# Performance work log

Measured on AMD Instinct MI355X. Metric: run time of the kernel, lower is better.

## Reference

```python
import jax, jax.numpy as jnp
import numpy as np

B, C, H, W = 32, 512, 32, 32  # in_dims = token_dim = 512, num_heads = 1
D = 512  # token_dim * num_heads
EPS = 1e-12  # torch F.normalize eps


def l2norm(x, axis):
    n = jnp.sqrt(jnp.sum(x * x, axis=axis, keepdims=True))
    return x / jnp.maximum(n, EPS)


def setup_inputs() -> dict:
    key = jax.random.key(0)
    ks = jax.random.split(key, 10)
    s = 1.0 / np.sqrt(D)
    return {
        "x_4d": jax.random.normal(ks[0], (B, C, H, W), dtype=jnp.float32),
        "Wq": jax.random.uniform(ks[1], (D, D), jnp.float32, -s, s),
        "bq": jax.random.uniform(ks[2], (D,), jnp.float32, -s, s),
        "Wk": jax.random.uniform(ks[3], (D, D), jnp.float32, -s, s),
        "bk": jax.random.uniform(ks[4], (D,), jnp.float32, -s, s),
        "w_g": jax.random.normal(ks[5], (D, 1), dtype=jnp.float32),
        "Wp": jax.random.uniform(ks[6], (D, D), jnp.float32, -s, s),
        "bp": jax.random.uniform(ks[7], (D,), jnp.float32, -s, s),
        "Wf": jax.random.uniform(ks[8], (D, D), jnp.float32, -s, s),
        "bf": jax.random.uniform(ks[9], (D,), jnp.float32, -s, s),
    }


def reference(x_4d, Wq, bq, Wk, bk, w_g, Wp, bp, Wf, bf):
    b, c, h, w = x_4d.shape
    n = h * w
    scale = D ** (-0.5)
    x = x_4d.reshape(b, c, n).transpose(0, 2, 1)  # [b, n, c]
    query = l2norm(jnp.einsum("bnc,dc->bnd", x, Wq) + bq, axis=-1)  # [b, n, d]
    key = l2norm(jnp.einsum("bnc,dc->bnd", x, Wk) + bk, axis=-1)    # [b, n, d]
    query_weight = query @ w_g                      # [b, n, 1]
    a = l2norm(query_weight * scale, axis=1)        # normalize over sequence dim
    g = jnp.sum(a * query, axis=1)                  # [b, d] global context
    out = jnp.einsum("bnd,ed->bne", g[:, None, :] * key, Wp) + bp + query
    out = jnp.einsum("bnd,ed->bne", out, Wf) + bf
    return out.transpose(0, 2, 1).reshape(b, c, h, w)
```

## Files before the change

kernel.cpp:

```cpp
#include <hip/hip_runtime.h>
#include <math.h>

#define B_ 32
#define D_ 512
#define N_ 1024
#define T_ 32768
#define SCALE 0.04419417382415922f

typedef unsigned short u16;
typedef __attribute__((ext_vector_type(8))) short bf16x8;
typedef __attribute__((ext_vector_type(4))) float f32x4;
typedef __attribute__((ext_vector_type(8))) unsigned short u16x8;

__device__ __forceinline__ u16 bf16_rn(float f) {
    unsigned u = __float_as_uint(f);
    u += 0x7FFFu + ((u >> 16) & 1u);
    return (u16)(u >> 16);
}
__device__ __forceinline__ float bf16f(u16 h) {
    return __uint_as_float(((unsigned)h) << 16);
}

__device__ __forceinline__ void g2l16(const u16* g, u16* lds) {
    __builtin_amdgcn_global_load_lds(
        (const __attribute__((address_space(1))) unsigned int*)g,
        (__attribute__((address_space(3))) unsigned int*)lds, 16, 0, 0);
}

__device__ __forceinline__ float waveRedSum(float v) {
#pragma unroll
    for (int off = 32; off > 0; off >>= 1) v += __shfl_xor(v, off, 64);
    return v;
}


__global__ __launch_bounds__(256) void convx_k(const float* __restrict__ x,
                                               u16* __restrict__ X) {
    __shared__ float tile[64][65];
    const int tid = threadIdx.x;
    const int n0 = blockIdx.x * 64, c0 = blockIdx.y * 64, b = blockIdx.z;
    const int nl = tid & 63, cl0 = (tid >> 6) * 16;
#pragma unroll
    for (int j = 0; j < 16; ++j)
        tile[cl0 + j][nl] = x[((size_t)(b * D_ + c0 + cl0 + j) << 10) + n0 + nl];
    __syncthreads();
    const int nr = tid >> 2, cb = (tid & 3) * 16;
    const size_t row = (size_t)(b * N_ + n0 + nr) * D_ + c0 + cb;
    u16 th[16];
#pragma unroll
    for (int j = 0; j < 16; ++j) th[j] = bf16_rn(tile[cb + j][nr]);
    *(u16x8*)&X[row]     = *(const u16x8*)&th[0];
    *(u16x8*)&X[row + 8] = *(const u16x8*)&th[8];
}

__global__ __launch_bounds__(256) void convw_k(const float* __restrict__ W0,
                                               const float* __restrict__ W1,
                                               const float* __restrict__ W2,
                                               u16* O0, u16* O1, u16* O2) {
    const int s = blockIdx.y;
    const float* src = (s == 0) ? W0 : ((s == 1) ? W1 : W2);
    u16* O = (s == 0) ? O0 : ((s == 1) ? O1 : O2);
    const size_t i0 = (size_t)blockIdx.x * 2048 + threadIdx.x * 8;
    u16 o[8];
#pragma unroll
    for (int j = 0; j < 8; ++j) o[j] = bf16_rn(src[i0 + j]);
    *(u16x8*)&O[i0] = *(const u16x8*)&o[0];
}

__global__ __launch_bounds__(256) void scalewp_k(const float* __restrict__ Wp,
                                                 const float* __restrict__ g,
                                                 u16* __restrict__ WpG) {
    const int b = blockIdx.y;
    const size_t f0 = (size_t)blockIdx.x * 2048 + threadIdx.x * 8;
    const int c = (int)(f0 & 511);
    u16 o[8];
#pragma unroll
    for (int j = 0; j < 8; ++j) o[j] = bf16_rn(Wp[f0 + j] * g[b * D_ + c + j]);
    *(u16x8*)&WpG[(size_t)b * 262144 + f0] = *(const u16x8*)&o[0];
}


__global__ __launch_bounds__(256) void rownorm_k(u16* __restrict__ Q,
                                                 u16* __restrict__ K,
                                                 const float* __restrict__ wg,
                                                 float* __restrict__ qw) {
    const int lane = threadIdx.x & 63;
    const int wv = threadIdx.x >> 6;
    const int row = blockIdx.x * 4 + wv;
    const int isK = blockIdx.y;
    u16* base = (isK ? K : Q) + (size_t)row * D_;
    u16x8 v = *(u16x8*)(base + lane * 8);
    float f[8];
    float ss = 0.f;
#pragma unroll
    for (int j = 0; j < 8; ++j) { f[j] = bf16f(v[j]); ss += f[j] * f[j]; }
    ss = waveRedSum(ss);
    const float sc = 1.f / fmaxf(sqrtf(ss), 1e-12f);
    u16 o[8];
#pragma unroll
    for (int j = 0; j < 8; ++j) o[j] = bf16_rn(f[j] * sc);
    *(u16x8*)(base + lane * 8) = *(const u16x8*)&o[0];
    if (!isK) {
        const float4 w0 = *(const float4*)(wg + lane * 8);
        const float4 w1 = *(const float4*)(wg + lane * 8 + 4);
        float d = f[0] * sc * w0.x + f[1] * sc * w0.y + f[2] * sc * w0.z +
                  f[3] * sc * w0.w + f[4] * sc * w1.x + f[5] * sc * w1.y +
                  f[6] * sc * w1.z + f[7] * sc * w1.w;
        d = waveRedSum(d);
        if (lane == 0) qw[row] = d;
    }
}

__global__ __launch_bounds__(256) void qwscale_k(float* __restrict__ qw) {
    __shared__ float red[4];
    const int b = blockIdx.x;
    float* p = qw + (size_t)b * N_ + threadIdx.x * 4;
    float4 v = *(float4*)p;
    float ss = v.x * v.x + v.y * v.y + v.z * v.z + v.w * v.w;
    ss = waveRedSum(ss);
    if ((threadIdx.x & 63) == 0) red[threadIdx.x >> 6] = ss;
    __syncthreads();
    const float S = red[0] + red[1] + red[2] + red[3];
    const float f = SCALE / fmaxf(SCALE * sqrtf(S), 1e-12f);
    v.x *= f; v.y *= f; v.z *= f; v.w *= f;
    *(float4*)p = v;
}

__global__ __launch_bounds__(512) void gctx_k(const float* __restrict__ qw,
                                              const u16* __restrict__ Qn,
                                              float* __restrict__ g) {
    const int b = blockIdx.y;
    const int n0 = blockIdx.x * 128;
    const int d = threadIdx.x;
    const u16* qp = Qn + ((size_t)b * N_ + n0) * D_ + d;
    const float* wp = qw + (size_t)b * N_ + n0;
    float acc = 0.f;
    for (int n = 0; n < 128; ++n) acc += wp[n] * bf16f(qp[(size_t)n * D_]);
    atomicAdd(g + b * D_ + d, acc);
}

template <int MODE>
__global__ __launch_bounds__(512) void mgemm(
        const u16* __restrict__ A, const u16* __restrict__ B0,
        const u16* __restrict__ B1,
        const float* __restrict__ bias0, const float* __restrict__ bias1,
        float* __restrict__ fout, u16* uout0, u16* uout1) {
    __shared__ u16 As[128 * 64];
    __shared__ u16 Bs[256 * 64];
    const int tid = threadIdx.x;
    const int l = tid & 63, w = tid >> 6;
    const int gid = blockIdx.x;
    const int xcd = gid & 7;

    int t0, e0, batch = 0;
    const u16* B;
    const float* bias;
    u16* uout = nullptr;
    if (MODE == 0) {
        const int bx = (gid >> 3) & 3;
        const int by = (gid >> 5) * 8 + xcd;
        t0 = by * 128;
        const bool sel = bx >= 2;
        e0 = (bx & 1) * 256;
        B = sel ? B1 : B0;
        bias = sel ? bias1 : bias0;
        uout = sel ? uout1 : uout0;
    } else if (MODE == 1) {
        const int bx = (gid >> 3) & 1;
        const int by = (gid >> 4) * 8 + xcd;
        t0 = by * 128; e0 = bx * 256; batch = by >> 3;
        B = B0 + (size_t)batch * 262144;
        bias = bias0;
        uout = uout0;
    } else {
        const int by = (gid >> 3) & 3;
        const int bx = (gid >> 5) * 8 + xcd;
        t0 = bx * 256; e0 = by * 128; batch = bx >> 2;
        B = B0;
        bias = bias0;
    }
    const int arow0 = (MODE == 2) ? e0 : t0;
    const int brow0 = (MODE == 2) ? t0 : e0;

    size_t gA[2], gB[4];
    u16 *ldsA[2], *ldsB[4];
#pragma unroll
    for (int i = 0; i < 2; ++i) {
        const int rr = w * 16 + i * 8 + (l >> 3);
        gA[i] = (size_t)(arow0 + rr) * 512 + (((l & 7) ^ (rr & 7)) * 8);
        ldsA[i] = As + (w * 16 + i * 8) * 64;
    }
#pragma unroll
    for (int i = 0; i < 4; ++i) {
        const int rr = w * 32 + i * 8 + (l >> 3);
        gB[i] = (size_t)(brow0 + rr) * 512 + (((l & 7) ^ (rr & 7)) * 8);
        ldsB[i] = Bs + (w * 32 + i * 8) * 64;
    }

    const int wr = w >> 2, wc = w & 3, kg = l >> 4, r16 = l & 15;
    int aoff[4][2], boff[4][2];
#pragma unroll
    for (int f = 0; f < 4; ++f)
#pragma unroll
        for (int h = 0; h < 2; ++h) {
            const int ra = wr * 64 + f * 16 + r16;
            aoff[f][h] = ra * 64 + (((h * 4 + kg) ^ (ra & 7)) * 8);
            const int rb = wc * 64 + f * 16 + r16;
            boff[f][h] = rb * 64 + (((h * 4 + kg) ^ (rb & 7)) * 8);
        }

    f32x4 acc[4][4];
#pragma unroll
    for (int i = 0; i < 4; ++i)
#pragma unroll
        for (int j = 0; j < 4; ++j) acc[i][j] = 0.f;

#pragma unroll 1
    for (int c0 = 0; c0 < 512; c0 += 64) {
        __syncthreads();
#pragma unroll
        for (int i = 0; i < 2; ++i) g2l16(A + gA[i] + c0, ldsA[i]);
#pragma unroll
        for (int i = 0; i < 4; ++i) g2l16(B + gB[i] + c0, ldsB[i]);
        __syncthreads();
#pragma unroll
        for (int h = 0; h < 2; ++h) {
            bf16x8 av[4], bv[4];
#pragma unroll
            for (int f = 0; f < 4; ++f) {
                av[f] = *(const bf16x8*)&As[aoff[f][h]];
                bv[f] = *(const bf16x8*)&Bs[boff[f][h]];
            }
#pragma unroll
            for (int i = 0; i < 4; ++i)
#pragma unroll
                for (int j = 0; j < 4; ++j)
                    acc[i][j] = __builtin_amdgcn_mfma_f32_16x16x32_bf16(
                        av[i], bv[j], acc[i][j], 0, 0, 0);
        }
    }

    const int mb = wr * 64 + kg * 4;
    const int nb = wc * 64 + r16;
    if (MODE == 2) {
#pragma unroll
        for (int fm = 0; fm < 4; ++fm)
#pragma unroll
            for (int fn = 0; fn < 4; ++fn) {
                const int ntok = (t0 & 1023) + nb + fn * 16;
#pragma unroll
                for (int q = 0; q < 4; ++q) {
                    const int e = e0 + mb + fm * 16 + q;
                    fout[((size_t)(batch * D_ + e) << 10) + ntok] =
                        acc[fm][fn][q] + bias[e];
                }
            }
    } else {
#pragma unroll
        for (int fm = 0; fm < 4; ++fm)
#pragma unroll
            for (int fn = 0; fn < 4; ++fn) {
                const int n = e0 + nb + fn * 16;
                const float bb = bias[n];
#pragma unroll
                for (int q = 0; q < 4; ++q) {
                    const int m = t0 + mb + fm * 16 + q;
                    const size_t idx = (size_t)m * 512 + n;
                    float val = acc[fm][fn][q] + bb;
                    if (MODE == 1) val += bf16f(uout[idx]);
                    uout[idx] = bf16_rn(val);
                }
            }
    }
}


extern "C" void kernel_launch(void* const* d_in, const int* in_sizes, int n_in,
                              void* d_out, int out_size, void* d_ws, size_t ws_size,
                              hipStream_t stream) {
    const float* x  = (const float*)d_in[0];
    const float* Wq = (const float*)d_in[1];
    const float* bq = (const float*)d_in[2];
    const float* Wk = (const float*)d_in[3];
    const float* bk = (const float*)d_in[4];
    const float* wg = (const float*)d_in[5];
    const float* Wp = (const float*)d_in[6];
    const float* bp = (const float*)d_in[7];
    const float* Wf = (const float*)d_in[8];
    const float* bf = (const float*)d_in[9];
    float* out = (float*)d_out;

    char* Wb = (char*)d_ws;
    u16* Xbf = (u16*)Wb;
    u16* WpG = (u16*)Wb;
    u16* Qn  = (u16*)(Wb + 33554432ull);
    u16* Kn  = (u16*)(Wb + 67108864ull);
    char* S  = Wb + 100663296ull;
    u16* Wqbf = (u16*)S;
    u16* Wkbf = (u16*)(S + 524288ull);
    u16* Wfbf = (u16*)(S + 1048576ull);
    float* QW = (float*)(S + 1572864ull);
    float* G  = (float*)(S + 1703936ull);

    const dim3 blk(256);

    convx_k<<<dim3(16, 8, 32), blk, 0, stream>>>(x, Xbf);
    convw_k<<<dim3(128, 3), blk, 0, stream>>>(Wq, Wk, Wf, Wqbf, Wkbf, Wfbf);
    mgemm<0><<<dim3(1024), dim3(512), 0, stream>>>(Xbf, Wqbf, Wkbf, bq, bk,
                                                   nullptr, Qn, Kn);
    rownorm_k<<<dim3(T_ / 4, 2), blk, 0, stream>>>(Qn, Kn, wg, QW);
    qwscale_k<<<dim3(B_), blk, 0, stream>>>(QW);
    hipMemsetAsync(G, 0, B_ * D_ * sizeof(float), stream);
    gctx_k<<<dim3(8, B_), dim3(512), 0, stream>>>(QW, Qn, G);
    scalewp_k<<<dim3(128, B_), blk, 0, stream>>>(Wp, G, WpG);
    mgemm<1><<<dim3(512), dim3(512), 0, stream>>>(Kn, WpG, nullptr, bp, nullptr,
                                                  nullptr, Qn, nullptr);
    mgemm<2><<<dim3(512), dim3(512), 0, stream>>>(Wfbf, Qn, nullptr, bf, nullptr,
                                                  out, nullptr, nullptr);
}
```

Before: 171.8 us.

## Fuse row L2-norm statistics into QK GEMM epilogue and defer normalization

```diff
diff --git a/kernel.cpp b/kernel.cpp
--- a/kernel.cpp
+++ b/kernel.cpp
@@ -67,63 +67,25 @@
     *(u16x8*)&O[i0] = *(const u16x8*)&o[0];
 }
 
-__global__ __launch_bounds__(256) void scalewp_k(const float* __restrict__ Wp,
-                                                 const float* __restrict__ g,
-                                                 u16* __restrict__ WpG) {
-    const int b = blockIdx.y;
-    const size_t f0 = (size_t)blockIdx.x * 2048 + threadIdx.x * 8;
-    const int c = (int)(f0 & 511);
-    u16 o[8];
-#pragma unroll
-    for (int j = 0; j < 8; ++j) o[j] = bf16_rn(Wp[f0 + j] * g[b * D_ + c + j]);
-    *(u16x8*)&WpG[(size_t)b * 262144 + f0] = *(const u16x8*)&o[0];
-}
-
-
-__global__ __launch_bounds__(256) void rownorm_k(u16* __restrict__ Q,
-                                                 u16* __restrict__ K,
-                                                 const float* __restrict__ wg,
-                                                 float* __restrict__ qw) {
-    const int lane = threadIdx.x & 63;
-    const int wv = threadIdx.x >> 6;
-    const int row = blockIdx.x * 4 + wv;
-    const int isK = blockIdx.y;
-    u16* base = (isK ? K : Q) + (size_t)row * D_;
-    u16x8 v = *(u16x8*)(base + lane * 8);
-    float f[8];
-    float ss = 0.f;
-#pragma unroll
-    for (int j = 0; j < 8; ++j) { f[j] = bf16f(v[j]); ss += f[j] * f[j]; }
-    ss = waveRedSum(ss);
-    const float sc = 1.f / fmaxf(sqrtf(ss), 1e-12f);
-    u16 o[8];
-#pragma unroll
-    for (int j = 0; j < 8; ++j) o[j] = bf16_rn(f[j] * sc);
-    *(u16x8*)(base + lane * 8) = *(const u16x8*)&o[0];
-    if (!isK) {
-        const float4 w0 = *(const float4*)(wg + lane * 8);
-        const float4 w1 = *(const float4*)(wg + lane * 8 + 4);
-        float d = f[0] * sc * w0.x + f[1] * sc * w0.y + f[2] * sc * w0.z +
-                  f[3] * sc * w0.w + f[4] * sc * w1.x + f[5] * sc * w1.y +
-                  f[6] * sc * w1.z + f[7] * sc * w1.w;
-        d = waveRedSum(d);
-        if (lane == 0) qw[row] = d;
-    }
-}
-
-__global__ __launch_bounds__(256) void qwscale_k(float* __restrict__ qw) {
+
+__global__ __launch_bounds__(256) void finalize_k(float* __restrict__ ssqQ,
+                                                  float* __restrict__ ssqK,
+                                                  float* __restrict__ qwr,
+                                                  float* __restrict__ Sb) {
     __shared__ float red[4];
-    const int b = blockIdx.x;
-    float* p = qw + (size_t)b * N_ + threadIdx.x * 4;
-    float4 v = *(float4*)p;
-    float ss = v.x * v.x + v.y * v.y + v.z * v.z + v.w * v.w;
-    ss = waveRedSum(ss);
-    if ((threadIdx.x & 63) == 0) red[threadIdx.x >> 6] = ss;
+    const int i = blockIdx.x * 256 + threadIdx.x;
+    const float rq = 1.f / fmaxf(sqrtf(ssqQ[i]), 1e-12f);
+    ssqQ[i] = rq;
+    const float rk = 1.f / fmaxf(sqrtf(ssqK[i]), 1e-12f);
+    ssqK[i] = rk;
+    const float qwp = qwr[i] * rq;
+    qwr[i] = qwp * rq;
+    float s = qwp * qwp;
+    s = waveRedSum(s);
+    if ((threadIdx.x & 63) == 0) red[threadIdx.x >> 6] = s;
     __syncthreads();
-    const float S = red[0] + red[1] + red[2] + red[3];
-    const float f = SCALE / fmaxf(SCALE * sqrtf(S), 1e-12f);
-    v.x *= f; v.y *= f; v.z *= f; v.w *= f;
-    *(float4*)p = v;
+    if (threadIdx.x == 0)
+        atomicAdd(Sb + (blockIdx.x >> 2), red[0] + red[1] + red[2] + red[3]);
 }
 
 __global__ __launch_bounds__(512) void gctx_k(const float* __restrict__ qw,
@@ -139,61 +101,56 @@
     atomicAdd(g + b * D_ + d, acc);
 }
 
-template <int MODE>
-__global__ __launch_bounds__(512) void mgemm(
+__global__ __launch_bounds__(256) void scalewp_k(const float* __restrict__ Wp,
+                                                 const float* __restrict__ g,
+                                                 const float* __restrict__ Sb,
+                                                 u16* __restrict__ WpG) {
+    const int b = blockIdx.y;
+    const float fb = SCALE / fmaxf(SCALE * sqrtf(Sb[b]), 1e-12f);
+    const size_t f0 = (size_t)blockIdx.x * 2048 + threadIdx.x * 8;
+    const int c = (int)(f0 & 511);
+    u16 o[8];
+#pragma unroll
+    for (int j = 0; j < 8; ++j)
+        o[j] = bf16_rn(Wp[f0 + j] * g[b * D_ + c + j] * fb);
+    *(u16x8*)&WpG[(size_t)b * 262144 + f0] = *(const u16x8*)&o[0];
+}
+
+__global__ __launch_bounds__(512) void mgemm0(
         const u16* __restrict__ A, const u16* __restrict__ B0,
         const u16* __restrict__ B1,
         const float* __restrict__ bias0, const float* __restrict__ bias1,
-        float* __restrict__ fout, u16* uout0, u16* uout1) {
+        const float* __restrict__ wg,
+        float* __restrict__ ssqQ, float* __restrict__ ssqK,
+        float* __restrict__ qwr, u16* uout0, u16* uout1) {
     __shared__ u16 As[128 * 64];
     __shared__ u16 Bs[256 * 64];
     const int tid = threadIdx.x;
     const int l = tid & 63, w = tid >> 6;
     const int gid = blockIdx.x;
     const int xcd = gid & 7;
-
-    int t0, e0, batch = 0;
-    const u16* B;
-    const float* bias;
-    u16* uout = nullptr;
-    if (MODE == 0) {
-        const int bx = (gid >> 3) & 3;
-        const int by = (gid >> 5) * 8 + xcd;
-        t0 = by * 128;
-        const bool sel = bx >= 2;
-        e0 = (bx & 1) * 256;
-        B = sel ? B1 : B0;
-        bias = sel ? bias1 : bias0;
-        uout = sel ? uout1 : uout0;
-    } else if (MODE == 1) {
-        const int bx = (gid >> 3) & 1;
-        const int by = (gid >> 4) * 8 + xcd;
-        t0 = by * 128; e0 = bx * 256; batch = by >> 3;
-        B = B0 + (size_t)batch * 262144;
-        bias = bias0;
-        uout = uout0;
-    } else {
-        const int by = (gid >> 3) & 3;
-        const int bx = (gid >> 5) * 8 + xcd;
-        t0 = bx * 256; e0 = by * 128; batch = bx >> 2;
-        B = B0;
-        bias = bias0;
-    }
-    const int arow0 = (MODE == 2) ? e0 : t0;
-    const int brow0 = (MODE == 2) ? t0 : e0;
+    const int bx = (gid >> 3) & 3;
+    const int by = (gid >> 5) * 8 + xcd;
+    const int t0 = by * 128;
+    const bool sel = bx >= 2;
+    const int e0 = (bx & 1) * 256;
+    const u16* B = sel ? B1 : B0;
+    const float* bias = sel ? bias1 : bias0;
+    u16* uout = sel ? uout1 : uout0;
+    float* ssq = sel ? ssqK : ssqQ;
 
     size_t gA[2], gB[4];
     u16 *ldsA[2], *ldsB[4];
 #pragma unroll
     for (int i = 0; i < 2; ++i) {
         const int rr = w * 16 + i * 8 + (l >> 3);
-        gA[i] = (size_t)(arow0 + rr) * 512 + (((l & 7) ^ (rr & 7)) * 8);
+        gA[i] = (size_t)(t0 + rr) * 512 + (((l & 7) ^ (rr & 7)) * 8);
         ldsA[i] = As + (w * 16 + i * 8) * 64;
     }
 #pragma unroll
     for (int i = 0; i < 4; ++i) {
         const int rr = w * 32 + i * 8 + (l >> 3);
-        gB[i] = (size_t)(brow0 + rr) * 512 + (((l & 7) ^ (rr & 7)) * 8);
+        gB[i] = (size_t)(e0 + rr) * 512 + (((l & 7) ^ (rr & 7)) * 8);
         ldsB[i] = Bs + (w * 32 + i * 8) * 64;
     }
 
@@ -242,33 +199,152 @@
 
     const int mb = wr * 64 + kg * 4;
     const int nb = wc * 64 + r16;
-    if (MODE == 2) {
+    float bb[4], wgv[4];
+#pragma unroll
+    for (int fn = 0; fn < 4; ++fn) {
+        const int n = e0 + nb + fn * 16;
+        bb[fn] = bias[n];
+        wgv[fn] = sel ? 0.f : wg[n];
+    }
+#pragma unroll
+    for (int fm = 0; fm < 4; ++fm) {
+#pragma unroll
+        for (int q = 0; q < 4; ++q) {
+            const int m = t0 + mb + fm * 16 + q;
+            float s2 = 0.f, wd = 0.f;
+#pragma unroll
+            for (int fn = 0; fn < 4; ++fn) {
+                const float val = acc[fm][fn][q] + bb[fn];
+                uout[(size_t)m * 512 + e0 + nb + fn * 16] = bf16_rn(val);
+                s2 += val * val;
+                wd += val * wgv[fn];
+            }
+#pragma unroll
+            for (int off = 1; off < 16; off <<= 1) {
+                s2 += __shfl_xor(s2, off, 64);
+                wd += __shfl_xor(wd, off, 64);
+            }
+            if (r16 == 0) {
+                atomicAdd(ssq + m, s2);
+                if (!sel) atomicAdd(qwr + m, wd);
+            }
+        }
+    }
+}
+
+template <int MODE>
+__global__ __launch_bounds__(256) void mgemm12(
+        const u16* __restrict__ A, const u16* __restrict__ B0,
+        const float* __restrict__ bias,
+        const float* __restrict__ rsA, const float* __restrict__ rsQ,
+        u16* uout, float* __restrict__ fout) {
+    __shared__ u16 As[128 * 64];
+    __shared__ u16 Bs[128 * 64];
+    const int tid = threadIdx.x;
+    const int l = tid & 63, w = tid >> 6;
+    const int gid = blockIdx.x;
+    const int xcd = gid & 7;
+    const int col = (gid >> 3) & 3;
+    const int rowt = (gid >> 5) * 8 + xcd;
+
+    const int t0 = rowt * 128 * (MODE == 1 ? 1 : 2) / (MODE == 1 ? 1 : 2);
+    const int tt0 = rowt * 128;
+    const int e0 = col * 128;
+    const int batch = rowt >> 3;
+    const u16* B = (MODE == 1) ? B0 + (size_t)batch * 262144 : B0;
+    const int arow0 = (MODE == 2) ? e0 : tt0;
+    const int brow0 = (MODE == 2) ? tt0 : e0;
+
+    size_t gA[4], gB[4];
+    u16 *ldsA[4], *ldsB[4];
+#pragma unroll
+    for (int i = 0; i < 4; ++i) {
+        const int rr = w * 32 + i * 8 + (l >> 3);
+        const int sw = ((l & 7) ^ (rr & 7)) * 8;
+        gA[i] = (size_t)(arow0 + rr) * 512 + sw;
+        gB[i] = (size_t)(brow0 + rr) * 512 + sw;
+        ldsA[i] = As + (w * 32 + i * 8) * 64;
+        ldsB[i] = Bs + (w * 32 + i * 8) * 64;
+    }
+
+    const int wr = w >> 1, wc = w & 1, kg = l >> 4, r16 = l & 15;
+    int aoff[4][2], boff[4][2];
+#pragma unroll
+    for (int f = 0; f < 4; ++f)
+#pragma unroll
+        for (int h = 0; h < 2; ++h) {
+            const int ra = wr * 64 + f * 16 + r16;
+            aoff[f][h] = ra * 64 + (((h * 4 + kg) ^ (ra & 7)) * 8);
+            const int rb = wc * 64 + f * 16 + r16;
+            boff[f][h] = rb * 64 + (((h * 4 + kg) ^ (rb & 7)) * 8);
+        }
+
+    f32x4 acc[4][4];
+#pragma unroll
+    for (int i = 0; i < 4; ++i)
+#pragma unroll
+        for (int j = 0; j < 4; ++j) acc[i][j] = 0.f;
+
+#pragma unroll 1
+    for (int c0 = 0; c0 < 512; c0 += 64) {
+        __syncthreads();
+#pragma unroll
+        for (int i = 0; i < 4; ++i) {
+            g2l16(A + gA[i] + c0, ldsA[i]);
+            g2l16(B + gB[i] + c0, ldsB[i]);
+        }
+        __syncthreads();
+#pragma unroll
+        for (int h = 0; h < 2; ++h) {
+            bf16x8 av[4], bv[4];
+#pragma unroll
+            for (int f = 0; f < 4; ++f) {
+                av[f] = *(const bf16x8*)&As[aoff[f][h]];
+                bv[f] = *(const bf16x8*)&Bs[boff[f][h]];
+            }
+#pragma unroll
+            for (int i = 0; i < 4; ++i)
+#pragma unroll
+                for (int j = 0; j < 4; ++j)
+                    acc[i][j] = __builtin_amdgcn_mfma_f32_16x16x32_bf16(
+                        av[i], bv[j], acc[i][j], 0, 0, 0);
+        }
+    }
+
+    const int mb = wr * 64 + kg * 4;
+    const int nb = wc * 64 + r16;
+    if (MODE == 1) {
+#pragma unroll
+        for (int fm = 0; fm < 4; ++fm) {
+            const int m0 = tt0 + mb + fm * 16;
+            const float4 ra4 = *(const float4*)(rsA + m0);
+            const float4 rq4 = *(const float4*)(rsQ + m0);
+            const float ra_[4] = {ra4.x, ra4.y, ra4.z, ra4.w};
+            const float rq_[4] = {rq4.x, rq4.y, rq4.z, rq4.w};
+#pragma unroll
+            for (int fn = 0; fn < 4; ++fn) {
+                const int n = e0 + nb + fn * 16;
+                const float bb = bias[n];
+#pragma unroll
+                for (int q = 0; q < 4; ++q) {
+                    const size_t idx = (size_t)(m0 + q) * 512 + n;
+                    const float val = acc[fm][fn][q] * ra_[q] + bb +
+                                      bf16f(uout[idx]) * rq_[q];
+                    uout[idx] = bf16_rn(val);
+                }
+            }
+        }
+    } else {
 #pragma unroll
         for (int fm = 0; fm < 4; ++fm)
 #pragma unroll
             for (int fn = 0; fn < 4; ++fn) {
-                const int ntok = (t0 & 1023) + nb + fn * 16;
+                const int ntok = (tt0 & 1023) + nb + fn * 16;
 #pragma unroll
                 for (int q = 0; q < 4; ++q) {
                     const int e = e0 + mb + fm * 16 + q;
                     fout[((size_t)(batch * D_ + e) << 10) + ntok] =
                         acc[fm][fn][q] + bias[e];
-                }
-            }
-    } else {
-#pragma unroll
-        for (int fm = 0; fm < 4; ++fm)
-#pragma unroll
-            for (int fn = 0; fn < 4; ++fn) {
-                const int n = e0 + nb + fn * 16;
-                const float bb = bias[n];
-#pragma unroll
-                for (int q = 0; q < 4; ++q) {
-                    const int m = t0 + mb + fm * 16 + q;
-                    const size_t idx = (size_t)m * 512 + n;
-                    float val = acc[fm][fn][q] + bb;
-                    if (MODE == 1) val += bf16f(uout[idx]);
-                    uout[idx] = bf16_rn(val);
                 }
             }
     }
@@ -299,22 +375,26 @@
     u16* Wqbf = (u16*)S;
     u16* Wkbf = (u16*)(S + 524288ull);
     u16* Wfbf = (u16*)(S + 1048576ull);
-    float* QW = (float*)(S + 1572864ull);
-    float* G  = (float*)(S + 1703936ull);
+    char* Z   = S + 1572864ull;
+    float* SSQQ = (float*)Z;
+    float* SSQK = (float*)(Z + 131072ull);
+    float* QWR  = (float*)(Z + 262144ull);
+    float* G    = (float*)(Z + 393216ull);
+    float* Sb   = (float*)(Z + 458752ull);
+    const size_t ZBYTES = 458752ull + 128ull;
 
     const dim3 blk(256);
 
     convx_k<<<dim3(16, 8, 32), blk, 0, stream>>>(x, Xbf);
     convw_k<<<dim3(128, 3), blk, 0, stream>>>(Wq, Wk, Wf, Wqbf, Wkbf, Wfbf);
-    mgemm<0><<<dim3(1024), dim3(512), 0, stream>>>(Xbf, Wqbf, Wkbf, bq, bk,
-                                                   nullptr, Qn, Kn);
-    rownorm_k<<<dim3(T_ / 4, 2), blk, 0, stream>>>(Qn, Kn, wg, QW);
-    qwscale_k<<<dim3(B_), blk, 0, stream>>>(QW);
-    hipMemsetAsync(G, 0, B_ * D_ * sizeof(float), stream);
-    gctx_k<<<dim3(8, B_), dim3(512), 0, stream>>>(QW, Qn, G);
-    scalewp_k<<<dim3(128, B_), blk, 0, stream>>>(Wp, G, WpG);
-    mgemm<1><<<dim3(512), dim3(512), 0, stream>>>(Kn, WpG, nullptr, bp, nullptr,
-                                                  nullptr, Qn, nullptr);
-    mgemm<2><<<dim3(512), dim3(512), 0, stream>>>(Wfbf, Qn, nullptr, bf, nullptr,
-                                                  out, nullptr, nullptr);
-}
+    hipMemsetAsync(Z, 0, ZBYTES, stream);
+    mgemm0<<<dim3(1024), dim3(512), 0, stream>>>(Xbf, Wqbf, Wkbf, bq, bk, wg,
+                                                 SSQQ, SSQK, QWR, Qn, Kn);
+    finalize_k<<<dim3(128), blk, 0, stream>>>(SSQQ, SSQK, QWR, Sb);
+    gctx_k<<<dim3(8, B_), dim3(512), 0, stream>>>(QWR, Qn, G);
+    scalewp_k<<<dim3(128, B_), blk, 0, stream>>>(Wp, G, Sb, WpG);
+    mgemm12<1><<<dim3(1024), blk, 0, stream>>>(Kn, WpG, bp, SSQK, SSQQ, Qn,
+                                               nullptr);
+    mgemm12<2><<<dim3(1024), blk, 0, stream>>>(Wfbf, Qn, bf, nullptr, nullptr,
+                                               nullptr, out);
+}
```

Result: faster. 157.1 us (-8.5%).
